# Kernel tuning notes

Measured on AMD Instinct MI355X. Metric: run time of the kernel, lower is better.

Reference implementation:

```python
import jax, jax.numpy as jnp
import numpy as np

B, N, L, D = 4, 128, 20, 512


def setup_inputs() -> dict:
    key = jax.random.key(0)
    ks = jax.random.split(key, 8)
    return {
        "f_b": jax.random.normal(ks[0], (B, N, D), jnp.float32),
        "f_w": jax.random.normal(ks[1], (B, L, D), jnp.float32),
        "f_s": jax.random.normal(ks[2], (B, D), jnp.float32),
        "f_m": jax.random.normal(ks[3], (B, N, N, D), jnp.float32),
        "Wq": jax.random.normal(ks[4], (D, D), jnp.float32) / np.sqrt(D).astype(np.float32),
        "bq": jax.random.normal(ks[5], (D,), jnp.float32) * 0.02,
        "Wk": jax.random.normal(ks[6], (D, D), jnp.float32) / np.sqrt(D).astype(np.float32),
        "bk": jax.random.normal(ks[7], (D,), jnp.float32) * 0.02,
    }


def reference(f_b, f_w, f_s, f_m, Wq, bq, Wk, bk):
    d = f_b.shape[-1]
    scale = jnp.asarray(1.0 / np.sqrt(d), f_b.dtype)
    # cross-attention: boundary features attend to word features
    q = f_b @ Wq.T + bq                                   # [B,N,D]
    k = f_w @ Wk.T + bk                                   # [B,L,D]
    attn = jax.nn.softmax(jnp.einsum('bnd,bld->bnl', q, k) * scale, axis=-1)
    f_baq = jnp.einsum('bnl,bld->bnd', attn, f_w)         # [B,N,D]
    # sentence-gated boundary features
    f_bq = f_b * (f_baq + f_s[:, None, :])                # [B,N,D]
    # boundary self-attention
    A_b = jax.nn.softmax(jnp.einsum('bnd,bmd->bnm', f_bq, f_bq) * scale, axis=-1)
    f_bb = jnp.einsum('bnm,bmd->bnd', A_b, f_b)           # [B,N,D]
    # gated moment-map reduction: sum_i A_b[b,i,j] * sigmoid(f_m*f_s)*f_m
    g_m = jax.nn.sigmoid(f_m * f_s[:, None, None, :])     # [B,N,N,D]
    f_bm = jnp.einsum('bij,bijd->bjd', A_b, g_m * f_m)    # [B,N,D]
    return f_bb + f_b + f_bm
```

## Files before the change

### kernel.cpp

```cpp
#include <hip/hip_runtime.h>
#include <hip/hip_bf16.h>

#define Bc 4
#define Nc 128
#define Lc 20
#define Dc 512
#define SCALE 0.04419417382415922f
#define NL2E -1.4426950408889634f

#if __has_builtin(__builtin_amdgcn_exp2f)
#define EXP2(x) __builtin_amdgcn_exp2f(x)
#else
#define EXP2(x) __expf((x) * 0.6931471805599453f)
#endif

__global__ __launch_bounds__(256)
void proj_gemm(const float* __restrict__ f_b, const float* __restrict__ f_w,
               const float* __restrict__ Wq, const float* __restrict__ bq,
               const float* __restrict__ Wk, const float* __restrict__ bk,
               float* __restrict__ qb, float* __restrict__ kb) {
    const int t  = threadIdx.x;
    const int tr = blockIdx.y, tc = blockIdx.x, kh = blockIdx.z;
    const int c0 = tc * 32;
    const bool isq = tr < 16;
    const float* Ain  = isq ? f_b : f_w;
    const float* W    = isq ? Wq : Wk;
    const float* bias = isq ? bq : bk;
    float* C          = isq ? (qb + kh * 512 * Dc) : (kb + kh * 80 * Dc);
    const int r0    = isq ? tr * 32 : (tr - 16) * 32;
    const int nrows = isq ? 512 : 80;
    const int kbase = kh * 128;

    __shared__ __align__(16) float As[16 * 34];
    __shared__ __align__(16) float Bs[16 * 34];

    const int sr  = t >> 3;
    const int sk2 = (t & 7) * 2;
    const int arow = min(r0 + sr, nrows - 1);
    const int wrow = c0 + sr;

    const int ty2 = (t >> 4) * 2;
    const int tx2 = (t & 15) * 2;
    float a00 = 0.f, a01 = 0.f, a10 = 0.f, a11 = 0.f;

    const float* Aptr = Ain + arow * Dc + kbase + sk2;
    const float* Wptr = W   + wrow * Dc + kbase + sk2;
    float2 ga = *(const float2*)Aptr;
    float2 gb = *(const float2*)Wptr;

    for (int kk0 = 16; kk0 <= 128; kk0 += 16) {
        __syncthreads();
        As[sk2 * 34 + sr]       = ga.x;
        As[(sk2 + 1) * 34 + sr] = ga.y;
        Bs[sk2 * 34 + sr]       = gb.x;
        Bs[(sk2 + 1) * 34 + sr] = gb.y;
        __syncthreads();
        if (kk0 < 128) {
            ga = *(const float2*)(Aptr + kk0);
            gb = *(const float2*)(Wptr + kk0);
        }
#pragma unroll
        for (int kk = 0; kk < 16; kk++) {
            const float2 av = *(const float2*)&As[kk * 34 + ty2];
            const float2 bv = *(const float2*)&Bs[kk * 34 + tx2];
            a00 = fmaf(av.x, bv.x, a00); a01 = fmaf(av.x, bv.y, a01);
            a10 = fmaf(av.y, bv.x, a10); a11 = fmaf(av.y, bv.y, a11);
        }
    }
    const int orow = r0 + ty2;
    const float b0 = kh ? 0.f : bias[c0 + tx2];
    const float b1 = kh ? 0.f : bias[c0 + tx2 + 1];
    if (orow < nrows)
        *(float2*)&C[orow * Dc + c0 + tx2] = make_float2(a00 + b0, a01 + b1);
    if (orow + 1 < nrows)
        *(float2*)&C[(orow + 1) * Dc + c0 + tx2] = make_float2(a10 + b0, a11 + b1);
}

__global__ __launch_bounds__(256)
void cross_attn_gate(const float* __restrict__ qb, const float* __restrict__ kb,
                     const float* __restrict__ f_w, const float* __restrict__ f_b,
                     const float* __restrict__ f_s, float* __restrict__ f_bq) {
    const int bn = blockIdx.x;
    const int b  = bn >> 7;
    const int t  = threadIdx.x;
    const int lane = t & 63, wave = t >> 6;

    __shared__ __align__(16) float qs[Dc];
    __shared__ float sc[32];
    __shared__ float invs;

    {
        float2 s = make_float2(0.f, 0.f);
#pragma unroll
        for (int h = 0; h < 4; h++) {
            const float2 u = ((const float2*)(qb + h * 512 * Dc + bn * Dc))[t];
            s.x += u.x; s.y += u.y;
        }
        ((float2*)qs)[t] = s;
    }
    __syncthreads();

    const float4* q4 = (const float4*)qs;
    const float4 qa = q4[lane];
    const float4 qv = q4[lane + 64];

    for (int l = wave; l < Lc; l += 4) {
        float4 ka = make_float4(0.f, 0.f, 0.f, 0.f);
        float4 kv = make_float4(0.f, 0.f, 0.f, 0.f);
#pragma unroll
        for (int h = 0; h < 4; h++) {
            const float4* kr = (const float4*)(kb + h * 80 * Dc + (b * Lc + l) * Dc);
            const float4 u = kr[lane];
            const float4 v = kr[lane + 64];
            ka.x += u.x; ka.y += u.y; ka.z += u.z; ka.w += u.w;
            kv.x += v.x; kv.y += v.y; kv.z += v.z; kv.w += v.w;
        }
        float s = qa.x * ka.x + qa.y * ka.y + qa.z * ka.z + qa.w * ka.w
                + qv.x * kv.x + qv.y * kv.y + qv.z * kv.z + qv.w * kv.w;
#pragma unroll
        for (int d = 32; d >= 1; d >>= 1) s += __shfl_down(s, d, 64);
        if (lane == 0) sc[l] = s * SCALE;
    }
    __syncthreads();

    if (t == 0) {
        float mx = sc[0];
        for (int l = 1; l < Lc; l++) mx = fmaxf(mx, sc[l]);
        float sum = 0.f;
        for (int l = 0; l < Lc; l++) { float e = __expf(sc[l] - mx); sc[l] = e; sum += e; }
        invs = 1.0f / sum;
    }
    __syncthreads();
    const float inv = invs;

    const float2* fw2 = (const float2*)(f_w + b * Lc * Dc);
    float2 acc = make_float2(0.f, 0.f);
#pragma unroll 5
    for (int l = 0; l < Lc; l++) {
        const float2 v = fw2[l * 256 + t];
        const float w = sc[l];
        acc.x = fmaf(w, v.x, acc.x);
        acc.y = fmaf(w, v.y, acc.y);
    }
    const float2 s2 = ((const float2*)(f_s + b * Dc))[t];
    const float2 fb2 = ((const float2*)(f_b + bn * Dc))[t];
    float2 o;
    o.x = fb2.x * (acc.x * inv + s2.x);
    o.y = fb2.y * (acc.y * inv + s2.y);
    ((float2*)(f_bq + bn * Dc))[t] = o;
}

__global__ __launch_bounds__(512)
void self_attn_scores(const float* __restrict__ f_bq,
                      float* __restrict__ A_b, float* __restrict__ A_bT) {
    const int bn = blockIdx.x;
    const int b  = bn >> 7, n = bn & 127;
    const int t  = threadIdx.x;
    const int lane = t & 63, wave = t >> 6;

    __shared__ __align__(16) float qrow[Dc];
    __shared__ float sc[Nc];
    __shared__ float red[Nc];

    qrow[t] = f_bq[bn * Dc + t];
    __syncthreads();

    const float4* q4 = (const float4*)qrow;
    const float4 qa = q4[lane];
    const float4 qv = q4[lane + 64];

    for (int m = wave; m < Nc; m += 8) {
        const float4* kr = (const float4*)(f_bq + (b * Nc + m) * Dc);
        const float4 va = kr[lane];
        const float4 vb = kr[lane + 64];
        float s = qa.x * va.x + qa.y * va.y + qa.z * va.z + qa.w * va.w
                + qv.x * vb.x + qv.y * vb.y + qv.z * vb.z + qv.w * vb.w;
#pragma unroll
        for (int d = 32; d >= 1; d >>= 1) s += __shfl_down(s, d, 64);
        if (lane == 0) sc[m] = s * SCALE;
    }
    __syncthreads();

    float e = 0.f, sval = 0.f;
    if (t < Nc) { sval = sc[t]; red[t] = sval; }
    __syncthreads();
    for (int st = 64; st >= 1; st >>= 1) {
        if (t < st) red[t] = fmaxf(red[t], red[t + st]);
        __syncthreads();
    }
    const float mx = red[0];
    __syncthreads();
    if (t < Nc) { e = __expf(sval - mx); red[t] = e; }
    __syncthreads();
    for (int st = 64; st >= 1; st >>= 1) {
        if (t < st) red[t] += red[t + st];
        __syncthreads();
    }
    if (t < Nc) {
        const float a = e * (1.0f / red[0]);
        A_b[bn * Nc + t] = a;
        A_bT[(b * Nc + t) * Nc + n] = a;
    }
}

__global__ __launch_bounds__(256, 8)
void moment_final(const float* __restrict__ f_m, const float* __restrict__ f_s,
                  const float* __restrict__ A_b, const float* __restrict__ A_bT,
                  const float* __restrict__ f_b, float* __restrict__ out) {
    const int bj = blockIdx.x;
    const int b  = bj >> 7, j = bj & 127;
    const int dq = blockIdx.y;
    const int t  = threadIdx.x;
    const int c  = t & 31;
    const int g  = t >> 5;

    __shared__ float w[Nc];
    __shared__ float ar[Nc];
    __shared__ __align__(16) float4 pex[7][32];

    if (t < Nc) w[t] = A_bT[bj * Nc + t];
    else        ar[t - Nc] = A_b[bj * Nc + (t - Nc)];
    __syncthreads();

    const int c4 = dq * 32 + c;
    const float4 s4 = ((const float4*)(f_s + b * Dc))[c4];
    const float4 ns = make_float4(NL2E * s4.x, NL2E * s4.y, NL2E * s4.z, NL2E * s4.w);

    float4 acc = make_float4(0.f, 0.f, 0.f, 0.f);
    const float4* fm4 = (const float4*)f_m;
    int idx = ((b * Nc + g * 16) * Nc + j) * (Dc / 4) + c4;

#pragma unroll 4
    for (int i = 0; i < 16; i++) {
        const float4 m4 = fm4[idx];
        idx += Nc * (Dc / 4);
        const float ww = w[g * 16 + i];
        acc.x = fmaf(ww * m4.x, __builtin_amdgcn_rcpf(1.f + EXP2(m4.x * ns.x)), acc.x);
        acc.y = fmaf(ww * m4.y, __builtin_amdgcn_rcpf(1.f + EXP2(m4.y * ns.y)), acc.y);
        acc.z = fmaf(ww * m4.z, __builtin_amdgcn_rcpf(1.f + EXP2(m4.z * ns.z)), acc.z);
        acc.w = fmaf(ww * m4.w, __builtin_amdgcn_rcpf(1.f + EXP2(m4.w * ns.w)), acc.w);
    }

    const float4* fb4 = (const float4*)(f_b + b * Nc * Dc);
#pragma unroll 4
    for (int m = g * 16; m < g * 16 + 16; m++) {
        const float a = ar[m];
        const float4 v = fb4[m * (Dc / 4) + c4];
        acc.x = fmaf(a, v.x, acc.x); acc.y = fmaf(a, v.y, acc.y);
        acc.z = fmaf(a, v.z, acc.z); acc.w = fmaf(a, v.w, acc.w);
    }

    if (g != 0) pex[g - 1][c] = acc;
    __syncthreads();
    if (g == 0) {
#pragma unroll
        for (int p = 0; p < 7; p++) {
            const float4 q = pex[p][c];
            acc.x += q.x; acc.y += q.y; acc.z += q.z; acc.w += q.w;
        }
        const float4 r = fb4[j * (Dc / 4) + c4];
        acc.x += r.x; acc.y += r.y; acc.z += r.z; acc.w += r.w;
        ((float4*)out)[bj * (Dc / 4) + c4] = acc;
    }
}

extern "C" void kernel_launch(void* const* d_in, const int* in_sizes, int n_in,
                              void* d_out, int out_size, void* d_ws, size_t ws_size,
                              hipStream_t stream) {
    const float* f_b = (const float*)d_in[0];
    const float* f_w = (const float*)d_in[1];
    const float* f_s = (const float*)d_in[2];
    const float* f_m = (const float*)d_in[3];
    const float* Wq  = (const float*)d_in[4];
    const float* bq  = (const float*)d_in[5];
    const float* Wk  = (const float*)d_in[6];
    const float* bk  = (const float*)d_in[7];
    float* out = (float*)d_out;

    float* ws   = (float*)d_ws;
    float* qb   = ws;
    float* kb   = qb   + 4 * 512 * Dc;
    float* f_bq = kb   + 4 * 80 * Dc;
    float* A_b  = f_bq + 512 * Dc;
    float* A_bT = A_b  + 512 * Nc;

    proj_gemm<<<dim3(16, 19, 4), 256, 0, stream>>>(f_b, f_w, Wq, bq, Wk, bk, qb, kb);
    cross_attn_gate<<<Bc * Nc, 256, 0, stream>>>(qb, kb, f_w, f_b, f_s, f_bq);
    self_attn_scores<<<Bc * Nc, 512, 0, stream>>>(f_bq, A_b, A_bT);
    moment_final<<<dim3(Bc * Nc, 4), 256, 0, stream>>>(f_m, f_s, A_b, A_bT, f_b, out);
}
```

Measured before the change: 242.8 us.

## Batch nontemporal f_m loads, widen moment tiles, use wave-shuffle softmax reductions

The moment reduction now has each block cover 256 columns with 4 groups of 32 rows, half the previous grid. Each thread issues 8 nontemporal float4 loads of f_m before computing on them, to raise memory-level parallelism on the dominant 128 MB stream. The self-attention softmax replaces the shared-memory tree reductions with wave shuffle reductions, cutting barriers. Risks: fewer blocks (1024) may reduce occupancy and latency hiding, and the higher register use is why launch bounds drop to 4 waves per SIMD.

```diff
diff --git a/kernel.cpp b/kernel.cpp
--- a/kernel.cpp
+++ b/kernel.cpp
@@ -12,6 +12,14 @@
 #define EXP2(x) __builtin_amdgcn_exp2f(x)
 #else
 #define EXP2(x) __expf((x) * 0.6931471805599453f)
+#endif
+
+typedef float vf4 __attribute__((ext_vector_type(4)));
+
+#if __has_builtin(__builtin_nontemporal_load)
+#define NT_LOAD4(p) __builtin_nontemporal_load((const vf4*)(p))
+#else
+#define NT_LOAD4(p) (*(const vf4*)(p))
 #endif
 
 __global__ __launch_bounds__(256)
@@ -160,7 +168,8 @@
 
     __shared__ __align__(16) float qrow[Dc];
     __shared__ float sc[Nc];
-    __shared__ float red[Nc];
+    __shared__ float redm[2];
+    __shared__ float reds[2];
 
     qrow[t] = f_bq[bn * Dc + t];
     __syncthreads();
@@ -181,69 +190,81 @@
     }
     __syncthreads();
 
-    float e = 0.f, sval = 0.f;
-    if (t < Nc) { sval = sc[t]; red[t] = sval; }
-    __syncthreads();
-    for (int st = 64; st >= 1; st >>= 1) {
-        if (t < st) red[t] = fmaxf(red[t], red[t + st]);
-        __syncthreads();
-    }
-    const float mx = red[0];
-    __syncthreads();
-    if (t < Nc) { e = __expf(sval - mx); red[t] = e; }
-    __syncthreads();
-    for (int st = 64; st >= 1; st >>= 1) {
-        if (t < st) red[t] += red[t + st];
-        __syncthreads();
-    }
+    float sval = 0.f, e = 0.f;
     if (t < Nc) {
-        const float a = e * (1.0f / red[0]);
+        sval = sc[t];
+        float m = sval;
+#pragma unroll
+        for (int d = 32; d >= 1; d >>= 1) m = fmaxf(m, __shfl_xor(m, d, 64));
+        if (lane == 0) redm[wave] = m;
+    }
+    __syncthreads();
+    if (t < Nc) {
+        const float mx = fmaxf(redm[0], redm[1]);
+        e = __expf(sval - mx);
+        float s = e;
+#pragma unroll
+        for (int d = 32; d >= 1; d >>= 1) s += __shfl_xor(s, d, 64);
+        if (lane == 0) reds[wave] = s;
+    }
+    __syncthreads();
+    if (t < Nc) {
+        const float a = e * (1.0f / (reds[0] + reds[1]));
         A_b[bn * Nc + t] = a;
         A_bT[(b * Nc + t) * Nc + n] = a;
     }
 }
 
-__global__ __launch_bounds__(256, 8)
+__global__ __launch_bounds__(256, 4)
 void moment_final(const float* __restrict__ f_m, const float* __restrict__ f_s,
                   const float* __restrict__ A_b, const float* __restrict__ A_bT,
                   const float* __restrict__ f_b, float* __restrict__ out) {
     const int bj = blockIdx.x;
     const int b  = bj >> 7, j = bj & 127;
-    const int dq = blockIdx.y;
+    const int dh = blockIdx.y;
     const int t  = threadIdx.x;
-    const int c  = t & 31;
-    const int g  = t >> 5;
+    const int c  = t & 63;
+    const int g  = t >> 6;
 
     __shared__ float w[Nc];
     __shared__ float ar[Nc];
-    __shared__ __align__(16) float4 pex[7][32];
+    __shared__ __align__(16) float4 pex[3][64];
 
     if (t < Nc) w[t] = A_bT[bj * Nc + t];
     else        ar[t - Nc] = A_b[bj * Nc + (t - Nc)];
     __syncthreads();
 
-    const int c4 = dq * 32 + c;
+    const int c4 = dh * 64 + c;
     const float4 s4 = ((const float4*)(f_s + b * Dc))[c4];
     const float4 ns = make_float4(NL2E * s4.x, NL2E * s4.y, NL2E * s4.z, NL2E * s4.w);
 
     float4 acc = make_float4(0.f, 0.f, 0.f, 0.f);
-    const float4* fm4 = (const float4*)f_m;
-    int idx = ((b * Nc + g * 16) * Nc + j) * (Dc / 4) + c4;
-
+    const float* fm = f_m;
+    const long istride = (long)Nc * Dc;
+    long idx = ((long)(b * Nc + g * 32) * Nc + j) * Dc + c4 * 4;
+
+#pragma unroll 1
+    for (int ii = 0; ii < 32; ii += 8) {
+        vf4 mv[8];
+#pragma unroll
+        for (int u = 0; u < 8; u++)
+            mv[u] = NT_LOAD4(fm + idx + (long)u * istride);
+        idx += 8 * istride;
+#pragma unroll
+        for (int u = 0; u < 8; u++) {
+            const float ww = w[g * 32 + ii + u];
+            const vf4 m4 = mv[u];
+            acc.x = fmaf(ww * m4.x, __builtin_amdgcn_rcpf(1.f + EXP2(m4.x * ns.x)), acc.x);
+            acc.y = fmaf(ww * m4.y, __builtin_amdgcn_rcpf(1.f + EXP2(m4.y * ns.y)), acc.y);
+            acc.z = fmaf(ww * m4.z, __builtin_amdgcn_rcpf(1.f + EXP2(m4.z * ns.z)), acc.z);
+            acc.w = fmaf(ww * m4.w, __builtin_amdgcn_rcpf(1.f + EXP2(m4.w * ns.w)), acc.w);
+        }
+    }
+
+    const float4* fb4 = (const float4*)(f_b + b * Nc * Dc);
+    const int mbase = g * 32;
 #pragma unroll 4
-    for (int i = 0; i < 16; i++) {
-        const float4 m4 = fm4[idx];
-        idx += Nc * (Dc / 4);
-        const float ww = w[g * 16 + i];
-        acc.x = fmaf(ww * m4.x, __builtin_amdgcn_rcpf(1.f + EXP2(m4.x * ns.x)), acc.x);
-        acc.y = fmaf(ww * m4.y, __builtin_amdgcn_rcpf(1.f + EXP2(m4.y * ns.y)), acc.y);
-        acc.z = fmaf(ww * m4.z, __builtin_amdgcn_rcpf(1.f + EXP2(m4.z * ns.z)), acc.z);
-        acc.w = fmaf(ww * m4.w, __builtin_amdgcn_rcpf(1.f + EXP2(m4.w * ns.w)), acc.w);
-    }
-
-    const float4* fb4 = (const float4*)(f_b + b * Nc * Dc);
-#pragma unroll 4
-    for (int m = g * 16; m < g * 16 + 16; m++) {
+    for (int m = mbase; m < mbase + 32; m++) {
         const float a = ar[m];
         const float4 v = fb4[m * (Dc / 4) + c4];
         acc.x = fmaf(a, v.x, acc.x); acc.y = fmaf(a, v.y, acc.y);
@@ -254,7 +275,7 @@
     __syncthreads();
     if (g == 0) {
 #pragma unroll
-        for (int p = 0; p < 7; p++) {
+        for (int p = 0; p < 3; p++) {
             const float4 q = pex[p][c];
             acc.x += q.x; acc.y += q.y; acc.z += q.z; acc.w += q.w;
         }
@@ -287,5 +308,5 @@
     proj_gemm<<<dim3(16, 19, 4), 256, 0, stream>>>(f_b, f_w, Wq, bq, Wk, bk, qb, kb);
     cross_attn_gate<<<Bc * Nc, 256, 0, stream>>>(qb, kb, f_w, f_b, f_s, f_bq);
     self_attn_scores<<<Bc * Nc, 512, 0, stream>>>(f_bq, A_b, A_bT);
-    moment_final<<<dim3(Bc * Nc, 4), 256, 0, stream>>>(f_m, f_s, A_b, A_bT, f_b, out);
-}
+    moment_final<<<dim3(Bc * Nc, 2), 256, 0, stream>>>(f_m, f_s, A_b, A_bT, f_b, out);
+}
```

After: 236.9 us. 1.02x faster.
